# Kernel tuning notes

Measured on AMD Instinct MI355X. Metric: run time of the kernel, lower is better.

Reference implementation:

```python
import jax, jax.numpy as jnp
import numpy as np

N = 50000
E = 800000
IN_DIM, HID, OUT_DIM = 768, 256, 128
BN_EPS = 1e-5
NORM_EPS = 1e-12


def setup_inputs() -> dict:
    key = jax.random.key(0)
    ks = jax.random.split(key, 16)
    inp = {
        "x": jax.random.normal(ks[0], (N, IN_DIM), dtype=jnp.float32),
        "edge_index": jax.random.randint(ks[1], (2, E), 0, N, dtype=jnp.int64),
        "edge_weight": jax.random.uniform(ks[2], (E,), dtype=jnp.float32),
        # GCNConv weights (PyG: out = scatter(norm * (x @ W)[src]) + b)
        "W1": jax.random.normal(ks[3], (IN_DIM, HID), dtype=jnp.float32) * 0.02,
        "b1": jnp.zeros((HID,), jnp.float32),
        "W2": jax.random.normal(ks[4], (HID, HID), dtype=jnp.float32) * 0.02,
        "b2": jnp.zeros((HID,), jnp.float32),
        "W3": jax.random.normal(ks[5], (HID, OUT_DIM), dtype=jnp.float32) * 0.02,
        "b3": jnp.zeros((OUT_DIM,), jnp.float32),
        # BatchNorm (eval mode: running stats)
        "bn1_gamma": jnp.ones((HID,), jnp.float32),
        "bn1_beta": jnp.zeros((HID,), jnp.float32),
        "bn1_mean": jax.random.normal(ks[6], (HID,), dtype=jnp.float32) * 0.1,
        "bn1_var": jax.random.uniform(ks[7], (HID,), dtype=jnp.float32) + 0.5,
        "bn2_gamma": jnp.ones((HID,), jnp.float32),
        "bn2_beta": jnp.zeros((HID,), jnp.float32),
        "bn2_mean": jax.random.normal(ks[8], (HID,), dtype=jnp.float32) * 0.1,
        "bn2_var": jax.random.uniform(ks[9], (HID,), dtype=jnp.float32) + 0.5,
    }
    return inp


def _gcn_norm(edge_index, edge_weight, n):
    # add self loops with weight 1 (PyG GCNConv default)
    src = jnp.concatenate([edge_index[0], jnp.arange(n, dtype=edge_index.dtype)])
    dst = jnp.concatenate([edge_index[1], jnp.arange(n, dtype=edge_index.dtype)])
    ew = jnp.concatenate([edge_weight, jnp.ones((n,), edge_weight.dtype)])
    deg = jax.ops.segment_sum(ew, dst, num_segments=n)  # [N]
    dis = jnp.where(deg > 0, jax.lax.rsqrt(deg), 0.0)
    norm = dis[src] * ew * dis[dst]  # [E+N]
    return src, dst, norm


def _gcn_conv(h, W, b, src, dst, norm, n):
    h = h @ W                                  # [N, F_out]
    msg = h[src] * norm[:, None]               # gather + scale, [E+N, F_out]
    out = jax.ops.segment_sum(msg, dst, num_segments=n)  # scatter-add
    return out + b


def _bn_eval(h, gamma, beta, mean, var):
    return (h - mean) * jax.lax.rsqrt(var + BN_EPS) * gamma + beta


def reference(x, edge_index, edge_weight,
              W1, b1, W2, b2, W3, b3,
              bn1_gamma, bn1_beta, bn1_mean, bn1_var,
              bn2_gamma, bn2_beta, bn2_mean, bn2_var):
    n = x.shape[0]
    src, dst, norm = _gcn_norm(edge_index, edge_weight, n)
    h = _gcn_conv(x, W1, b1, src, dst, norm, n)
    h = jax.nn.relu(_bn_eval(h, bn1_gamma, bn1_beta, bn1_mean, bn1_var))
    h = _gcn_conv(h, W2, b2, src, dst, norm, n)
    h = jax.nn.relu(_bn_eval(h, bn2_gamma, bn2_beta, bn2_mean, bn2_var))
    h = _gcn_conv(h, W3, b3, src, dst, norm, n)
    # F.normalize(x, p=2, dim=1): x / max(||x||, eps)
    nrm = jnp.sqrt(jnp.sum(h * h, axis=1, keepdims=True))
    return h / jnp.maximum(nrm, NORM_EPS)
```

## Files before the change

kernel.cpp:

```cpp
#include <hip/hip_runtime.h>
#include <cstddef>

#define NN 50000
#define EE 800000
#define NB 196

typedef __attribute__((ext_vector_type(8))) _Float16 f16x8;
typedef __attribute__((ext_vector_type(4))) _Float16 f16x4;
typedef __attribute__((ext_vector_type(2))) _Float16 f16x2;
typedef __attribute__((ext_vector_type(4))) float f32x4;

__device__ __forceinline__ unsigned pk2h(float a, float b) {
  auto h = __builtin_amdgcn_cvt_pkrtz(a, b);
  return __builtin_bit_cast(unsigned, h);
}

__global__ void k_zero_off(int* __restrict__ off) {
  int i = blockIdx.x * 256 + threadIdx.x;
  if (i <= NN) off[i] = 0;
}

__global__ void k_count(const int* __restrict__ src, const int* __restrict__ dst,
                        int* __restrict__ off) {
  int e = blockIdx.x * 256 + threadIdx.x;
  if (e < EE) {
    int s = src[e], d = dst[e];
    if (s >= 0 && s < NN && d >= 0 && d < NN) atomicAdd(&off[d], 1);
  }
}

__global__ void k_scanA(int* __restrict__ off, int* __restrict__ bsum) {
  __shared__ int sh[256];
  int t = threadIdx.x;
  int idx = blockIdx.x * 256 + t;
  int v = (idx < NN) ? off[idx] : 0;
  sh[t] = v;
  __syncthreads();
  for (int d = 1; d < 256; d <<= 1) {
    int x = (t >= d) ? sh[t - d] : 0;
    __syncthreads();
    sh[t] += x;
    __syncthreads();
  }
  if (idx < NN) off[idx] = sh[t] - v;
  if (t == 255) bsum[blockIdx.x] = sh[255];
}

__global__ void k_scanB(int* __restrict__ bsum, int* __restrict__ bpre,
                        int* __restrict__ off) {
  __shared__ int sh[256];
  int t = threadIdx.x;
  int v = (t < NB) ? bsum[t] : 0;
  sh[t] = v;
  __syncthreads();
  for (int d = 1; d < 256; d <<= 1) {
    int x = (t >= d) ? sh[t - d] : 0;
    __syncthreads();
    sh[t] += x;
    __syncthreads();
  }
  if (t < NB) bpre[t] = sh[t] - v;
  if (t == 255) off[NN] = sh[255];
}

__global__ void k_scanC(int* __restrict__ off, const int* __restrict__ bpre,
                        int* __restrict__ cursor) {
  int idx = blockIdx.x * 256 + threadIdx.x;
  if (idx < NN) {
    int o = off[idx] + bpre[blockIdx.x];
    off[idx] = o;
    cursor[idx] = o;
  }
}

__global__ void k_fill(const int* __restrict__ src, const int* __restrict__ dst,
                       const float* __restrict__ ew, int* __restrict__ cursor,
                       int* __restrict__ csrc, float* __restrict__ cew) {
  int e = blockIdx.x * 256 + threadIdx.x;
  if (e < EE) {
    int s = src[e], d = dst[e];
    if (s >= 0 && s < NN && d >= 0 && d < NN) {
      int p = atomicAdd(&cursor[d], 1);
      csrc[p] = s;
      cew[p] = ew[e];
    }
  }
}

__global__ void k_degdis(const int* __restrict__ off, const float* __restrict__ cew,
                         float* __restrict__ dis) {
  int i = blockIdx.x * 256 + threadIdx.x;
  if (i >= NN) return;
  int e0 = off[i], e1 = off[i + 1];
  float s = 1.0f;
  for (int e = e0; e < e1; ++e) s += cew[e];
  dis[i] = rsqrtf(s);
}

__global__ void k_affine(const float* __restrict__ g1, const float* __restrict__ be1,
                         const float* __restrict__ m1, const float* __restrict__ v1,
                         const float* __restrict__ g2, const float* __restrict__ be2,
                         const float* __restrict__ m2, const float* __restrict__ v2,
                         float* __restrict__ s1, float* __restrict__ u1,
                         float* __restrict__ s2, float* __restrict__ u2) {
  int f = threadIdx.x;
  float a1 = g1[f] * rsqrtf(v1[f] + 1e-5f);
  s1[f] = a1; u1[f] = be1[f] - m1[f] * a1;
  float a2 = g2[f] * rsqrtf(v2[f] + 1e-5f);
  s2[f] = a2; u2[f] = be2[f] - m2[f] * a2;
}

__global__ void k_wt(const float* __restrict__ W, _Float16* __restrict__ WT,
                     int K, int N) {
  int k = blockIdx.x * 256 + threadIdx.x;
  int n = blockIdx.y;
  if (k < K) WT[(size_t)n * K + k] = (_Float16)W[(size_t)k * N + n];
}

#define LDA 40
__global__ __launch_bounds__(256) void k_gemm_mfma(const void* __restrict__ Ain,
                                                   const _Float16* __restrict__ BT,
                                                   _Float16* __restrict__ C,
                                                   int M, int K, int Nout, int a_fp32) {
  __shared__ _Float16 As[128 * LDA];
  __shared__ _Float16 Bs[128 * LDA];
  const int tid = threadIdx.x;
  const int bm = blockIdx.y << 7;
  const int bn = blockIdx.x << 7;
  const int lane = tid & 63;
  const int wid = tid >> 6;
  const int wm = (wid & 1) << 6;
  const int wn = (wid >> 1) << 6;
  const int quad = lane >> 4;
  const int l16 = lane & 15;

  f32x4 acc[4][4] = {};

  for (int k0 = 0; k0 < K; k0 += 32) {
#pragma unroll
    for (int j = 0; j < 2; ++j) {
      int c = tid + (j << 8);
      int row = c >> 2, kc = c & 3;
      uint4 va = make_uint4(0, 0, 0, 0);
      int gr = bm + row;
      if (gr < M) {
        if (a_fp32) {
          const float* p = (const float*)Ain + (size_t)gr * K + k0 + (kc << 3);
          float4 f0 = *(const float4*)p;
          float4 f1 = *(const float4*)(p + 4);
          va.x = pk2h(f0.x, f0.y);
          va.y = pk2h(f0.z, f0.w);
          va.z = pk2h(f1.x, f1.y);
          va.w = pk2h(f1.z, f1.w);
        } else {
          va = *(const uint4*)((const _Float16*)Ain + (size_t)gr * K + k0 + (kc << 3));
        }
      }
      *(uint4*)&As[row * LDA + (kc << 3)] = va;
      uint4 vb = *(const uint4*)(BT + (size_t)(bn + row) * K + k0 + (kc << 3));
      *(uint4*)&Bs[row * LDA + (kc << 3)] = vb;
    }
    __syncthreads();
    f16x8 af[4], bfr[4];
#pragma unroll
    for (int mt = 0; mt < 4; ++mt)
      af[mt] = *(const f16x8*)&As[(wm + (mt << 4) + l16) * LDA + (quad << 3)];
#pragma unroll
    for (int nt = 0; nt < 4; ++nt)
      bfr[nt] = *(const f16x8*)&Bs[(wn + (nt << 4) + l16) * LDA + (quad << 3)];
#pragma unroll
    for (int mt = 0; mt < 4; ++mt)
#pragma unroll
      for (int nt = 0; nt < 4; ++nt)
        acc[mt][nt] = __builtin_amdgcn_mfma_f32_16x16x32_f16(af[mt], bfr[nt], acc[mt][nt], 0, 0, 0);
    __syncthreads();
  }

  const int rbase = bm + wm + (quad << 2);
#pragma unroll
  for (int mt = 0; mt < 4; ++mt) {
#pragma unroll
    for (int reg = 0; reg < 4; ++reg) {
      int r = rbase + (mt << 4) + reg;
      if (r < M) {
        _Float16* crow = C + (size_t)r * Nout + bn + wn + l16;
#pragma unroll
        for (int nt = 0; nt < 4; ++nt) crow[nt << 4] = (_Float16)acc[mt][nt][reg];
      }
    }
  }
}

__global__ __launch_bounds__(256) void k_agg256(const _Float16* __restrict__ hW,
                                                const float* __restrict__ dis,
                                                const float* __restrict__ b,
                                                const int* __restrict__ off,
                                                const int* __restrict__ csrc,
                                                const float* __restrict__ cew,
                                                const float* __restrict__ s,
                                                const float* __restrict__ u,
                                                _Float16* __restrict__ hout) {
  int i = (blockIdx.x << 2) + (threadIdx.x >> 6);
  if (i >= NN) return;
  int lane = threadIdx.x & 63;
  float di = dis[i];
  float4 bb = *(const float4*)(b + (lane << 2));
  f16x4 hv = *(const f16x4*)(hW + (size_t)i * 256 + (lane << 2));
  float d2 = di * di;
  float4 acc;
  acc.x = fmaf((float)hv.x, d2, bb.x);
  acc.y = fmaf((float)hv.y, d2, bb.y);
  acc.z = fmaf((float)hv.z, d2, bb.z);
  acc.w = fmaf((float)hv.w, d2, bb.w);
  int e0 = off[i], e1 = off[i + 1];
  int e = e0;
  for (; e + 3 < e1; e += 4) {
    int sa = csrc[e], sb = csrc[e + 1], sc = csrc[e + 2], sd = csrc[e + 3];
    float wa = dis[sa] * cew[e] * di;
    float wb = dis[sb] * cew[e + 1] * di;
    float wc = dis[sc] * cew[e + 2] * di;
    float wd = dis[sd] * cew[e + 3] * di;
    f16x4 ra = *(const f16x4*)(hW + (size_t)sa * 256 + (lane << 2));
    f16x4 rb = *(const f16x4*)(hW + (size_t)sb * 256 + (lane << 2));
    f16x4 rc = *(const f16x4*)(hW + (size_t)sc * 256 + (lane << 2));
    f16x4 rd = *(const f16x4*)(hW + (size_t)sd * 256 + (lane << 2));
    acc.x = fmaf((float)ra.x, wa, acc.x); acc.y = fmaf((float)ra.y, wa, acc.y);
    acc.z = fmaf((float)ra.z, wa, acc.z); acc.w = fmaf((float)ra.w, wa, acc.w);
    acc.x = fmaf((float)rb.x, wb, acc.x); acc.y = fmaf((float)rb.y, wb, acc.y);
    acc.z = fmaf((float)rb.z, wb, acc.z); acc.w = fmaf((float)rb.w, wb, acc.w);
    acc.x = fmaf((float)rc.x, wc, acc.x); acc.y = fmaf((float)rc.y, wc, acc.y);
    acc.z = fmaf((float)rc.z, wc, acc.z); acc.w = fmaf((float)rc.w, wc, acc.w);
    acc.x = fmaf((float)rd.x, wd, acc.x); acc.y = fmaf((float)rd.y, wd, acc.y);
    acc.z = fmaf((float)rd.z, wd, acc.z); acc.w = fmaf((float)rd.w, wd, acc.w);
  }
  for (; e < e1; ++e) {
    int sa = csrc[e];
    float wa = dis[sa] * cew[e] * di;
    f16x4 ra = *(const f16x4*)(hW + (size_t)sa * 256 + (lane << 2));
    acc.x = fmaf((float)ra.x, wa, acc.x); acc.y = fmaf((float)ra.y, wa, acc.y);
    acc.z = fmaf((float)ra.z, wa, acc.z); acc.w = fmaf((float)ra.w, wa, acc.w);
  }
  float4 sv = *(const float4*)(s + (lane << 2));
  float4 uv = *(const float4*)(u + (lane << 2));
  float r0 = fmaxf(fmaf(acc.x, sv.x, uv.x), 0.f);
  float r1 = fmaxf(fmaf(acc.y, sv.y, uv.y), 0.f);
  float r2 = fmaxf(fmaf(acc.z, sv.z, uv.z), 0.f);
  float r3 = fmaxf(fmaf(acc.w, sv.w, uv.w), 0.f);
  uint2 pk;
  pk.x = pk2h(r0, r1);
  pk.y = pk2h(r2, r3);
  *(uint2*)&hout[(size_t)i * 256 + (lane << 2)] = pk;
}

__global__ __launch_bounds__(256) void k_agg128_l2(const _Float16* __restrict__ hW,
                                                   const float* __restrict__ dis,
                                                   const float* __restrict__ b,
                                                   const int* __restrict__ off,
                                                   const int* __restrict__ csrc,
                                                   const float* __restrict__ cew,
                                                   float* __restrict__ out) {
  int i = (blockIdx.x << 2) + (threadIdx.x >> 6);
  if (i >= NN) return;
  int lane = threadIdx.x & 63;
  float di = dis[i];
  float2 bb = *(const float2*)(b + (lane << 1));
  f16x2 hv = *(const f16x2*)(hW + (size_t)i * 128 + (lane << 1));
  float d2 = di * di;
  float2 acc;
  acc.x = fmaf((float)hv.x, d2, bb.x);
  acc.y = fmaf((float)hv.y, d2, bb.y);
  int e0 = off[i], e1 = off[i + 1];
  int e = e0;
  for (; e + 3 < e1; e += 4) {
    int sa = csrc[e], sb = csrc[e + 1], sc = csrc[e + 2], sd = csrc[e + 3];
    float wa = dis[sa] * cew[e] * di;
    float wb = dis[sb] * cew[e + 1] * di;
    float wc = dis[sc] * cew[e + 2] * di;
    float wd = dis[sd] * cew[e + 3] * di;
    f16x2 ra = *(const f16x2*)(hW + (size_t)sa * 128 + (lane << 1));
    f16x2 rb = *(const f16x2*)(hW + (size_t)sb * 128 + (lane << 1));
    f16x2 rc = *(const f16x2*)(hW + (size_t)sc * 128 + (lane << 1));
    f16x2 rd = *(const f16x2*)(hW + (size_t)sd * 128 + (lane << 1));
    acc.x = fmaf((float)ra.x, wa, acc.x); acc.y = fmaf((float)ra.y, wa, acc.y);
    acc.x = fmaf((float)rb.x, wb, acc.x); acc.y = fmaf((float)rb.y, wb, acc.y);
    acc.x = fmaf((float)rc.x, wc, acc.x); acc.y = fmaf((float)rc.y, wc, acc.y);
    acc.x = fmaf((float)rd.x, wd, acc.x); acc.y = fmaf((float)rd.y, wd, acc.y);
  }
  for (; e < e1; ++e) {
    int sa = csrc[e];
    float wa = dis[sa] * cew[e] * di;
    f16x2 ra = *(const f16x2*)(hW + (size_t)sa * 128 + (lane << 1));
    acc.x = fmaf((float)ra.x, wa, acc.x); acc.y = fmaf((float)ra.y, wa, acc.y);
  }
  float ss = fmaf(acc.x, acc.x, acc.y * acc.y);
#pragma unroll
  for (int o = 32; o > 0; o >>= 1) ss += __shfl_xor(ss, o, 64);
  float sc2 = 1.0f / fmaxf(sqrtf(ss), 1e-12f);
  acc.x *= sc2;
  acc.y *= sc2;
  *(float2*)(out + (size_t)i * 128 + (lane << 1)) = acc;
}

extern "C" void kernel_launch(void* const* d_in, const int* in_sizes, int n_in,
                              void* d_out, int out_size, void* d_ws, size_t ws_size,
                              hipStream_t stream) {
  const size_t OFF_CUR = 50176, OFF_BS = 100352, OFF_BP = 100608;
  const size_t OFF_CS = 100864, OFF_CW = 900864, OFF_DIS = 1700864;
  const size_t OFF_AFF = 1751040, OFF_HW = 1752064;
  const size_t OFF_HB = OFF_HW + (size_t)NN * 256;
  const size_t OFF_WT1 = OFF_HB + (size_t)NN * 128;
  const size_t OFF_WT2 = OFF_WT1 + 768 * 256 / 2;
  const size_t OFF_WT3 = OFF_WT2 + 256 * 256 / 2;
  const size_t WS_UNITS = OFF_WT3 + 256 * 128 / 2 + 256;
  if (ws_size < WS_UNITS * 4) return;

  const float* x  = (const float*)d_in[0];
  const int* ei   = (const int*)d_in[1];
  const float* ew = (const float*)d_in[2];
  const float* W1 = (const float*)d_in[3];
  const float* b1 = (const float*)d_in[4];
  const float* W2 = (const float*)d_in[5];
  const float* b2 = (const float*)d_in[6];
  const float* W3 = (const float*)d_in[7];
  const float* b3 = (const float*)d_in[8];
  const float* g1 = (const float*)d_in[9];
  const float* be1 = (const float*)d_in[10];
  const float* m1 = (const float*)d_in[11];
  const float* v1 = (const float*)d_in[12];
  const float* g2 = (const float*)d_in[13];
  const float* be2 = (const float*)d_in[14];
  const float* m2 = (const float*)d_in[15];
  const float* v2 = (const float*)d_in[16];
  float* out = (float*)d_out;
  const int* src = ei;
  const int* dstp = ei + EE;

  int* wsi = (int*)d_ws;
  float* wsf = (float*)d_ws;
  int* off = wsi;
  int* cursor = wsi + OFF_CUR;
  int* bsum = wsi + OFF_BS;
  int* bpre = wsi + OFF_BP;
  int* csrc = wsi + OFF_CS;
  float* cew = wsf + OFF_CW;
  float* dis = wsf + OFF_DIS;
  float* s1 = wsf + OFF_AFF;
  float* u1 = s1 + 256;
  float* s2 = u1 + 256;
  float* u2 = s2 + 256;
  _Float16* hW = (_Float16*)(wsf + OFF_HW);
  _Float16* hb = (_Float16*)(wsi + OFF_HB);
  _Float16* wT1 = (_Float16*)(wsi + OFF_WT1);
  _Float16* wT2 = (_Float16*)(wsi + OFF_WT2);
  _Float16* wT3 = (_Float16*)(wsi + OFF_WT3);

  dim3 b256(256);
  const int EB = (EE + 255) / 256;
  k_zero_off<<<NB, b256, 0, stream>>>(off);
  k_count<<<EB, b256, 0, stream>>>(src, dstp, off);
  k_scanA<<<NB, b256, 0, stream>>>(off, bsum);
  k_scanB<<<1, b256, 0, stream>>>(bsum, bpre, off);
  k_scanC<<<NB, b256, 0, stream>>>(off, bpre, cursor);
  k_fill<<<EB, b256, 0, stream>>>(src, dstp, ew, cursor, csrc, cew);
  k_degdis<<<NB, b256, 0, stream>>>(off, cew, dis);
  k_affine<<<1, b256, 0, stream>>>(g1, be1, m1, v1, g2, be2, m2, v2, s1, u1, s2, u2);
  k_wt<<<dim3(3, 256), b256, 0, stream>>>(W1, wT1, 768, 256);
  k_wt<<<dim3(1, 256), b256, 0, stream>>>(W2, wT2, 256, 256);
  k_wt<<<dim3(1, 128), b256, 0, stream>>>(W3, wT3, 256, 128);

  const int GM = (NN + 127) / 128;
  const int AGB = (NN + 3) / 4;
  k_gemm_mfma<<<dim3(2, GM), b256, 0, stream>>>(x, wT1, hW, NN, 768, 256, 1);
  k_agg256<<<AGB, b256, 0, stream>>>(hW, dis, b1, off, csrc, cew, s1, u1, hb);
  k_gemm_mfma<<<dim3(2, GM), b256, 0, stream>>>(hb, wT2, hW, NN, 256, 256, 0);
  k_agg256<<<AGB, b256, 0, stream>>>(hW, dis, b2, off, csrc, cew, s2, u2, hb);
  k_gemm_mfma<<<dim3(1, GM), b256, 0, stream>>>(hb, wT3, hW, NN, 256, 128, 0);
  k_agg128_l2<<<AGB, b256, 0, stream>>>(hW, dis, b3, off, csrc, cew, out);
}
```

Baseline: 633.2 us.

## Halve GEMM M-tile and prefetch next K-slice into registers

The MFMA GEMM tile shrinks from 128x128 to 64x128 rows per block, doubling the grid so more blocks are resident. The main loop also becomes software-pipelined: the next K-slice of A and B is loaded into registers while MFMAs run on the current LDS tile, then stored to LDS after a barrier. The aim is to hide global-load latency and raise occupancy. The cost is an extra barrier per iteration, less B-tile reuse per block, and more global traffic for B.

```diff
diff --git a/kernel.cpp b/kernel.cpp
--- a/kernel.cpp
+++ b/kernel.cpp
@@ -122,63 +122,92 @@
                                                    const _Float16* __restrict__ BT,
                                                    _Float16* __restrict__ C,
                                                    int M, int K, int Nout, int a_fp32) {
-  __shared__ _Float16 As[128 * LDA];
+  __shared__ _Float16 As[64 * LDA];
   __shared__ _Float16 Bs[128 * LDA];
   const int tid = threadIdx.x;
-  const int bm = blockIdx.y << 7;
+  const int bm = blockIdx.y << 6;
   const int bn = blockIdx.x << 7;
   const int lane = tid & 63;
   const int wid = tid >> 6;
-  const int wm = (wid & 1) << 6;
+  const int wm = (wid & 1) << 5;
   const int wn = (wid >> 1) << 6;
   const int quad = lane >> 4;
   const int l16 = lane & 15;
 
-  f32x4 acc[4][4] = {};
-
-  for (int k0 = 0; k0 < K; k0 += 32) {
-#pragma unroll
-    for (int j = 0; j < 2; ++j) {
-      int c = tid + (j << 8);
-      int row = c >> 2, kc = c & 3;
-      uint4 va = make_uint4(0, 0, 0, 0);
-      int gr = bm + row;
-      if (gr < M) {
+  const int srow = tid >> 2, skc = tid & 3;
+  const int agr = bm + srow;
+  const int aok = (agr < M);
+  const _Float16* brow0 = BT + (size_t)(bn + srow) * K + (skc << 3);
+  const _Float16* brow1 = BT + (size_t)(bn + 64 + srow) * K + (skc << 3);
+
+  f32x4 acc[2][4] = {};
+  uint4 ra, rb0, rb1;
+
+  const int T = K >> 5;
+
+  {
+    ra = make_uint4(0, 0, 0, 0);
+    if (aok) {
+      if (a_fp32) {
+        const float* p = (const float*)Ain + (size_t)agr * K + (skc << 3);
+        float4 f0 = *(const float4*)p;
+        float4 f1 = *(const float4*)(p + 4);
+        ra.x = pk2h(f0.x, f0.y); ra.y = pk2h(f0.z, f0.w);
+        ra.z = pk2h(f1.x, f1.y); ra.w = pk2h(f1.z, f1.w);
+      } else {
+        ra = *(const uint4*)((const _Float16*)Ain + (size_t)agr * K + (skc << 3));
+      }
+    }
+    rb0 = *(const uint4*)brow0;
+    rb1 = *(const uint4*)brow1;
+  }
+  *(uint4*)&As[srow * LDA + (skc << 3)] = ra;
+  *(uint4*)&Bs[srow * LDA + (skc << 3)] = rb0;
+  *(uint4*)&Bs[(64 + srow) * LDA + (skc << 3)] = rb1;
+  __syncthreads();
+
+  for (int t = 0; t < T; ++t) {
+    if (t + 1 < T) {
+      int k0 = (t + 1) << 5;
+      ra = make_uint4(0, 0, 0, 0);
+      if (aok) {
         if (a_fp32) {
-          const float* p = (const float*)Ain + (size_t)gr * K + k0 + (kc << 3);
+          const float* p = (const float*)Ain + (size_t)agr * K + k0 + (skc << 3);
           float4 f0 = *(const float4*)p;
           float4 f1 = *(const float4*)(p + 4);
-          va.x = pk2h(f0.x, f0.y);
-          va.y = pk2h(f0.z, f0.w);
-          va.z = pk2h(f1.x, f1.y);
-          va.w = pk2h(f1.z, f1.w);
+          ra.x = pk2h(f0.x, f0.y); ra.y = pk2h(f0.z, f0.w);
+          ra.z = pk2h(f1.x, f1.y); ra.w = pk2h(f1.z, f1.w);
         } else {
-          va = *(const uint4*)((const _Float16*)Ain + (size_t)gr * K + k0 + (kc << 3));
+          ra = *(const uint4*)((const _Float16*)Ain + (size_t)agr * K + k0 + (skc << 3));
         }
       }
-      *(uint4*)&As[row * LDA + (kc << 3)] = va;
-      uint4 vb = *(const uint4*)(BT + (size_t)(bn + row) * K + k0 + (kc << 3));
-      *(uint4*)&Bs[row * LDA + (kc << 3)] = vb;
+      rb0 = *(const uint4*)(brow0 + k0);
+      rb1 = *(const uint4*)(brow1 + k0);
     }
-    __syncthreads();
-    f16x8 af[4], bfr[4];
-#pragma unroll
-    for (int mt = 0; mt < 4; ++mt)
+    f16x8 af[2], bfr[4];
+#pragma unroll
+    for (int mt = 0; mt < 2; ++mt)
       af[mt] = *(const f16x8*)&As[(wm + (mt << 4) + l16) * LDA + (quad << 3)];
 #pragma unroll
     for (int nt = 0; nt < 4; ++nt)
       bfr[nt] = *(const f16x8*)&Bs[(wn + (nt << 4) + l16) * LDA + (quad << 3)];
 #pragma unroll
-    for (int mt = 0; mt < 4; ++mt)
+    for (int mt = 0; mt < 2; ++mt)
 #pragma unroll
       for (int nt = 0; nt < 4; ++nt)
         acc[mt][nt] = __builtin_amdgcn_mfma_f32_16x16x32_f16(af[mt], bfr[nt], acc[mt][nt], 0, 0, 0);
     __syncthreads();
+    if (t + 1 < T) {
+      *(uint4*)&As[srow * LDA + (skc << 3)] = ra;
+      *(uint4*)&Bs[srow * LDA + (skc << 3)] = rb0;
+      *(uint4*)&Bs[(64 + srow) * LDA + (skc << 3)] = rb1;
+    }
+    __syncthreads();
   }
 
   const int rbase = bm + wm + (quad << 2);
 #pragma unroll
-  for (int mt = 0; mt < 4; ++mt) {
+  for (int mt = 0; mt < 2; ++mt) {
 #pragma unroll
     for (int reg = 0; reg < 4; ++reg) {
       int r = rbase + (mt << 4) + reg;
@@ -368,7 +397,7 @@
   k_wt<<<dim3(1, 256), b256, 0, stream>>>(W2, wT2, 256, 256);
   k_wt<<<dim3(1, 128), b256, 0, stream>>>(W3, wT3, 256, 128);
 
-  const int GM = (NN + 127) / 128;
+  const int GM = (NN + 63) / 64;
   const int AGB = (NN + 3) / 4;
   k_gemm_mfma<<<dim3(2, GM), b256, 0, stream>>>(x, wT1, hW, NN, 768, 256, 1);
   k_agg256<<<AGB, b256, 0, stream>>>(hW, dis, b1, off, csrc, cew, s1, u1, hb);
```

Measured after the change: 602.3 us. 1.05x faster.

## Double-buffer GEMM shared tiles with register prefetch and shrink M tile to 64

Applied to the files above, without the earlier changes.

The MFMA GEMM now uses double-buffered shared-memory tiles. Global loads for the next K-slice are issued into registers before the current slice is computed and written to the other buffer afterwards, so load latency overlaps with MFMA work. The M tile shrinks from 128 to 64 rows, which doubles the block count and raises occupancy. The fp32/fp16 A path is now a template parameter instead of a runtime flag. In exchange, each block reuses the B tile across fewer rows, so more B traffic is re-read from L2, and more registers are held for the prefetch.

```diff
diff --git a/kernel.cpp b/kernel.cpp
--- a/kernel.cpp
+++ b/kernel.cpp
@@ -118,67 +118,108 @@
 }
 
 #define LDA 40
-__global__ __launch_bounds__(256) void k_gemm_mfma(const void* __restrict__ Ain,
-                                                   const _Float16* __restrict__ BT,
-                                                   _Float16* __restrict__ C,
-                                                   int M, int K, int Nout, int a_fp32) {
-  __shared__ _Float16 As[128 * LDA];
-  __shared__ _Float16 Bs[128 * LDA];
+template <int A32>
+__global__ __launch_bounds__(256) void k_gemm(const void* __restrict__ Ain,
+                                              const _Float16* __restrict__ BT,
+                                              _Float16* __restrict__ C,
+                                              int M, int K, int Nout) {
+  __shared__ _Float16 As[2][64 * LDA];
+  __shared__ _Float16 Bs[2][128 * LDA];
   const int tid = threadIdx.x;
-  const int bm = blockIdx.y << 7;
+  const int bm = blockIdx.y << 6;
   const int bn = blockIdx.x << 7;
   const int lane = tid & 63;
   const int wid = tid >> 6;
-  const int wm = (wid & 1) << 6;
+  const int wm = (wid & 1) << 5;
   const int wn = (wid >> 1) << 6;
   const int quad = lane >> 4;
   const int l16 = lane & 15;
 
-  f32x4 acc[4][4] = {};
-
-  for (int k0 = 0; k0 < K; k0 += 32) {
-#pragma unroll
-    for (int j = 0; j < 2; ++j) {
-      int c = tid + (j << 8);
-      int row = c >> 2, kc = c & 3;
-      uint4 va = make_uint4(0, 0, 0, 0);
-      int gr = bm + row;
-      if (gr < M) {
-        if (a_fp32) {
-          const float* p = (const float*)Ain + (size_t)gr * K + k0 + (kc << 3);
-          float4 f0 = *(const float4*)p;
-          float4 f1 = *(const float4*)(p + 4);
-          va.x = pk2h(f0.x, f0.y);
-          va.y = pk2h(f0.z, f0.w);
-          va.z = pk2h(f1.x, f1.y);
-          va.w = pk2h(f1.z, f1.w);
-        } else {
-          va = *(const uint4*)((const _Float16*)Ain + (size_t)gr * K + k0 + (kc << 3));
-        }
-      }
-      *(uint4*)&As[row * LDA + (kc << 3)] = va;
-      uint4 vb = *(const uint4*)(BT + (size_t)(bn + row) * K + k0 + (kc << 3));
-      *(uint4*)&Bs[row * LDA + (kc << 3)] = vb;
+  const int srow = tid >> 2, skc = tid & 3;
+  const int agr = bm + srow;
+  const int aok = (agr < M);
+  const _Float16* ap16 = (const _Float16*)Ain + (size_t)agr * K + (skc << 3);
+  const float* ap32 = (const float*)Ain + (size_t)agr * K + (skc << 3);
+  const _Float16* bp0 = BT + (size_t)(bn + srow) * K + (skc << 3);
+  const _Float16* bp1 = BT + (size_t)(bn + 64 + srow) * K + (skc << 3);
+
+  f32x4 acc[2][4] = {};
+
+  uint4 a16_0, a16_1;
+  float4 a32lo_0, a32hi_0, a32lo_1, a32hi_1;
+  uint4 b0_0, b1_0, b0_1, b1_1;
+
+#define ISSUE(S, k0)                                                        \
+  do {                                                                      \
+    if (A32) {                                                              \
+      if (aok) {                                                            \
+        a32lo_##S = *(const float4*)(ap32 + (k0));                          \
+        a32hi_##S = *(const float4*)(ap32 + (k0) + 4);                      \
+      } else {                                                              \
+        a32lo_##S = make_float4(0.f, 0.f, 0.f, 0.f);                       \
+        a32hi_##S = make_float4(0.f, 0.f, 0.f, 0.f);                       \
+      }                                                                     \
+    } else {                                                                \
+      a16_##S = aok ? *(const uint4*)(ap16 + (k0)) : make_uint4(0, 0, 0, 0);\
+    }                                                                       \
+    b0_##S = *(const uint4*)(bp0 + (k0));                                   \
+    b1_##S = *(const uint4*)(bp1 + (k0));                                   \
+  } while (0)
+
+#define COMMIT(S, buf)                                                      \
+  do {                                                                      \
+    uint4 va;                                                               \
+    if (A32) {                                                              \
+      va.x = pk2h(a32lo_##S.x, a32lo_##S.y);                                \
+      va.y = pk2h(a32lo_##S.z, a32lo_##S.w);                                \
+      va.z = pk2h(a32hi_##S.x, a32hi_##S.y);                                \
+      va.w = pk2h(a32hi_##S.z, a32hi_##S.w);                                \
+    } else {                                                                \
+      va = a16_##S;                                                         \
+    }                                                                       \
+    *(uint4*)&As[buf][srow * LDA + (skc << 3)] = va;                        \
+    *(uint4*)&Bs[buf][srow * LDA + (skc << 3)] = b0_##S;                    \
+    *(uint4*)&Bs[buf][(64 + srow) * LDA + (skc << 3)] = b1_##S;             \
+  } while (0)
+
+#define COMPUTE(buf)                                                        \
+  do {                                                                      \
+    f16x8 af[2], bfr[4];                                                    \
+    _Pragma("unroll") for (int mt = 0; mt < 2; ++mt)                        \
+        af[mt] = *(const f16x8*)&As[buf][(wm + (mt << 4) + l16) * LDA + (quad << 3)]; \
+    _Pragma("unroll") for (int nt = 0; nt < 4; ++nt)                        \
+        bfr[nt] = *(const f16x8*)&Bs[buf][(wn + (nt << 4) + l16) * LDA + (quad << 3)]; \
+    _Pragma("unroll") for (int mt = 0; mt < 2; ++mt)                        \
+        _Pragma("unroll") for (int nt = 0; nt < 4; ++nt)                    \
+            acc[mt][nt] = __builtin_amdgcn_mfma_f32_16x16x32_f16(af[mt], bfr[nt], acc[mt][nt], 0, 0, 0); \
+  } while (0)
+
+  const int T = K >> 5;
+
+  ISSUE(0, 0);
+  COMMIT(0, 0);
+  if (T > 1) ISSUE(1, 32);
+  __syncthreads();
+
+  for (int t = 0; t < T; t += 2) {
+    if (t + 2 < T) ISSUE(0, (t + 2) << 5);
+    COMPUTE(0);
+    if (t + 1 < T) COMMIT(1, 1);
+    __syncthreads();
+    if (t + 1 < T) {
+      if (t + 3 < T) ISSUE(1, (t + 3) << 5);
+      COMPUTE(1);
+      if (t + 2 < T) COMMIT(0, 0);
+      __syncthreads();
     }
-    __syncthreads();
-    f16x8 af[4], bfr[4];
-#pragma unroll
-    for (int mt = 0; mt < 4; ++mt)
-      af[mt] = *(const f16x8*)&As[(wm + (mt << 4) + l16) * LDA + (quad << 3)];
-#pragma unroll
-    for (int nt = 0; nt < 4; ++nt)
-      bfr[nt] = *(const f16x8*)&Bs[(wn + (nt << 4) + l16) * LDA + (quad << 3)];
-#pragma unroll
-    for (int mt = 0; mt < 4; ++mt)
-#pragma unroll
-      for (int nt = 0; nt < 4; ++nt)
-        acc[mt][nt] = __builtin_amdgcn_mfma_f32_16x16x32_f16(af[mt], bfr[nt], acc[mt][nt], 0, 0, 0);
-    __syncthreads();
-  }
+  }
+#undef ISSUE
+#undef COMMIT
+#undef COMPUTE
 
   const int rbase = bm + wm + (quad << 2);
 #pragma unroll
-  for (int mt = 0; mt < 4; ++mt) {
+  for (int mt = 0; mt < 2; ++mt) {
 #pragma unroll
     for (int reg = 0; reg < 4; ++reg) {
       int r = rbase + (mt << 4) + reg;
@@ -368,12 +409,12 @@
   k_wt<<<dim3(1, 256), b256, 0, stream>>>(W2, wT2, 256, 256);
   k_wt<<<dim3(1, 128), b256, 0, stream>>>(W3, wT3, 256, 128);
 
-  const int GM = (NN + 127) / 128;
+  const int GM = (NN + 63) / 64;
   const int AGB = (NN + 3) / 4;
-  k_gemm_mfma<<<dim3(2, GM), b256, 0, stream>>>(x, wT1, hW, NN, 768, 256, 1);
+  k_gemm<1><<<dim3(2, GM), b256, 0, stream>>>(x, wT1, hW, NN, 768, 256);
   k_agg256<<<AGB, b256, 0, stream>>>(hW, dis, b1, off, csrc, cew, s1, u1, hb);
-  k_gemm_mfma<<<dim3(2, GM), b256, 0, stream>>>(hb, wT2, hW, NN, 256, 256, 0);
+  k_gemm<0><<<dim3(2, GM), b256, 0, stream>>>(hb, wT2, hW, NN, 256, 256);
   k_agg256<<<AGB, b256, 0, stream>>>(hW, dis, b2, off, csrc, cew, s2, u2, hb);
-  k_gemm_mfma<<<dim3(1, GM), b256, 0, stream>>>(hb, wT3, hW, NN, 256, 128, 0);
+  k_gemm<0><<<dim3(1, GM), b256, 0, stream>>>(hb, wT3, hW, NN, 256, 128);
   k_agg128_l2<<<AGB, b256, 0, stream>>>(hW, dis, b3, off, csrc, cew, out);
 }
```

Measured after the change: 608.8 us. -3.9%, faster.

## Replace LDS-tiled GEMM with register-direct double-buffered MFMA loads

Applied to the files above, without the earlier changes.

The GEMM drops shared-memory staging and its barriers. Each wave now loads its A and B fragments directly from global memory into registers, with two-stage software double-buffering, and computes a 32x64 tile per wave (128x64 per block). The fp32/fp16 A path becomes a template parameter. This removes the LDS round-trip and __syncthreads, but B and A are reloaded from global/L2 by each wave with less reuse, and the grid doubles in the N dimension, which re-reads x across more blocks.

```diff
diff --git a/kernel.cpp b/kernel.cpp
--- a/kernel.cpp
+++ b/kernel.cpp
@@ -117,73 +117,90 @@
   if (k < K) WT[(size_t)n * K + k] = (_Float16)W[(size_t)k * N + n];
 }
 
-#define LDA 40
-__global__ __launch_bounds__(256) void k_gemm_mfma(const void* __restrict__ Ain,
-                                                   const _Float16* __restrict__ BT,
-                                                   _Float16* __restrict__ C,
-                                                   int M, int K, int Nout, int a_fp32) {
-  __shared__ _Float16 As[128 * LDA];
-  __shared__ _Float16 Bs[128 * LDA];
+template <int A32>
+__global__ __launch_bounds__(256) void k_gemm(const void* __restrict__ Ain,
+                                              const _Float16* __restrict__ BT,
+                                              _Float16* __restrict__ C,
+                                              int M, int K, int Nout) {
   const int tid = threadIdx.x;
-  const int bm = blockIdx.y << 7;
-  const int bn = blockIdx.x << 7;
   const int lane = tid & 63;
   const int wid = tid >> 6;
-  const int wm = (wid & 1) << 6;
-  const int wn = (wid >> 1) << 6;
+  const int bm = (blockIdx.y << 7) + (wid << 5);
+  const int bn = blockIdx.x << 6;
   const int quad = lane >> 4;
   const int l16 = lane & 15;
 
-  f32x4 acc[4][4] = {};
-
-  for (int k0 = 0; k0 < K; k0 += 32) {
+  const int r0 = bm + l16, r1 = bm + 16 + l16;
+  const size_t a0 = (size_t)(r0 < M ? r0 : 0) * K + (quad << 3);
+  const size_t a1 = (size_t)(r1 < M ? r1 : 0) * K + (quad << 3);
+  const float* ap32_0 = (const float*)Ain + a0;
+  const float* ap32_1 = (const float*)Ain + a1;
+  const _Float16* ap16_0 = (const _Float16*)Ain + a0;
+  const _Float16* ap16_1 = (const _Float16*)Ain + a1;
+  const _Float16* bp0 = BT + (size_t)(bn + l16) * K + (quad << 3);
+  const _Float16* bp1 = BT + (size_t)(bn + 16 + l16) * K + (quad << 3);
+  const _Float16* bp2 = BT + (size_t)(bn + 32 + l16) * K + (quad << 3);
+  const _Float16* bp3 = BT + (size_t)(bn + 48 + l16) * K + (quad << 3);
+
+  f32x4 acc[2][4] = {};
+
+  f16x8 af0_0, af1_0, bf0_0, bf1_0, bf2_0, bf3_0;
+  f16x8 af0_1, af1_1, bf0_1, bf1_1, bf2_1, bf3_1;
+
+#define LOADF(S, k0)                                                          \
+  do {                                                                        \
+    if (A32) {                                                                \
+      const float* p0 = ap32_0 + (k0);                                        \
+      const float* p1 = ap32_1 + (k0);                                        \
+      float4 u0 = *(const float4*)p0, v0 = *(const float4*)(p0 + 4);          \
+      float4 u1 = *(const float4*)p1, v1 = *(const float4*)(p1 + 4);          \
+      af0_##S = __builtin_bit_cast(f16x8,                                     \
+          make_uint4(pk2h(u0.x, u0.y), pk2h(u0.z, u0.w),                      \
+                     pk2h(v0.x, v0.y), pk2h(v0.z, v0.w)));                    \
+      af1_##S = __builtin_bit_cast(f16x8,                                     \
+          make_uint4(pk2h(u1.x, u1.y), pk2h(u1.z, u1.w),                      \
+                     pk2h(v1.x, v1.y), pk2h(v1.z, v1.w)));                    \
+    } else {                                                                  \
+      af0_##S = *(const f16x8*)(ap16_0 + (k0));                               \
+      af1_##S = *(const f16x8*)(ap16_1 + (k0));                               \
+    }                                                                         \
+    bf0_##S = *(const f16x8*)(bp0 + (k0));                                    \
+    bf1_##S = *(const f16x8*)(bp1 + (k0));                                    \
+    bf2_##S = *(const f16x8*)(bp2 + (k0));                                    \
+    bf3_##S = *(const f16x8*)(bp3 + (k0));                                    \
+  } while (0)
+
+#define MSTEP(S)                                                              \
+  do {                                                                        \
+    acc[0][0] = __builtin_amdgcn_mfma_f32_16x16x32_f16(af0_##S, bf0_##S, acc[0][0], 0, 0, 0); \
+    acc[0][1] = __builtin_amdgcn_mfma_f32_16x16x32_f16(af0_##S, bf1_##S, acc[0][1], 0, 0, 0); \
+    acc[0][2] = __builtin_amdgcn_mfma_f32_16x16x32_f16(af0_##S, bf2_##S, acc[0][2], 0, 0, 0); \
+    acc[0][3] = __builtin_amdgcn_mfma_f32_16x16x32_f16(af0_##S, bf3_##S, acc[0][3], 0, 0, 0); \
+    acc[1][0] = __builtin_amdgcn_mfma_f32_16x16x32_f16(af1_##S, bf0_##S, acc[1][0], 0, 0, 0); \
+    acc[1][1] = __builtin_amdgcn_mfma_f32_16x16x32_f16(af1_##S, bf1_##S, acc[1][1], 0, 0, 0); \
+    acc[1][2] = __builtin_amdgcn_mfma_f32_16x16x32_f16(af1_##S, bf2_##S, acc[1][2], 0, 0, 0); \
+    acc[1][3] = __builtin_amdgcn_mfma_f32_16x16x32_f16(af1_##S, bf3_##S, acc[1][3], 0, 0, 0); \
+  } while (0)
+
+  const int T = K >> 5;
+  LOADF(0, 0);
+  for (int t = 0; t < T; t += 2) {
+    if (t + 1 < T) LOADF(1, (t + 1) << 5);
+    MSTEP(0);
+    if (t + 2 < T) LOADF(0, (t + 2) << 5);
+    if (t + 1 < T) MSTEP(1);
+  }
+#undef LOADF
+#undef MSTEP
+
+  const int rbase = bm + (quad << 2);
 #pragma unroll
-    for (int j = 0; j < 2; ++j) {
-      int c = tid + (j << 8);
-      int row = c >> 2, kc = c & 3;
-      uint4 va = make_uint4(0, 0, 0, 0);
-      int gr = bm + row;
-      if (gr < M) {
-        if (a_fp32) {
-          const float* p = (const float*)Ain + (size_t)gr * K + k0 + (kc << 3);
-          float4 f0 = *(const float4*)p;
-          float4 f1 = *(const float4*)(p + 4);
-          va.x = pk2h(f0.x, f0.y);
-          va.y = pk2h(f0.z, f0.w);
-          va.z = pk2h(f1.x, f1.y);
-          va.w = pk2h(f1.z, f1.w);
-        } else {
-          va = *(const uint4*)((const _Float16*)Ain + (size_t)gr * K + k0 + (kc << 3));
-        }
-      }
-      *(uint4*)&As[row * LDA + (kc << 3)] = va;
-      uint4 vb = *(const uint4*)(BT + (size_t)(bn + row) * K + k0 + (kc << 3));
-      *(uint4*)&Bs[row * LDA + (kc << 3)] = vb;
-    }
-    __syncthreads();
-    f16x8 af[4], bfr[4];
-#pragma unroll
-    for (int mt = 0; mt < 4; ++mt)
-      af[mt] = *(const f16x8*)&As[(wm + (mt << 4) + l16) * LDA + (quad << 3)];
-#pragma unroll
-    for (int nt = 0; nt < 4; ++nt)
-      bfr[nt] = *(const f16x8*)&Bs[(wn + (nt << 4) + l16) * LDA + (quad << 3)];
-#pragma unroll
-    for (int mt = 0; mt < 4; ++mt)
-#pragma unroll
-      for (int nt = 0; nt < 4; ++nt)
-        acc[mt][nt] = __builtin_amdgcn_mfma_f32_16x16x32_f16(af[mt], bfr[nt], acc[mt][nt], 0, 0, 0);
-    __syncthreads();
-  }
-
-  const int rbase = bm + wm + (quad << 2);
-#pragma unroll
-  for (int mt = 0; mt < 4; ++mt) {
+  for (int mt = 0; mt < 2; ++mt) {
 #pragma unroll
     for (int reg = 0; reg < 4; ++reg) {
       int r = rbase + (mt << 4) + reg;
       if (r < M) {
-        _Float16* crow = C + (size_t)r * Nout + bn + wn + l16;
+        _Float16* crow = C + (size_t)r * Nout + bn + l16;
 #pragma unroll
         for (int nt = 0; nt < 4; ++nt) crow[nt << 4] = (_Float16)acc[mt][nt][reg];
       }
@@ -370,10 +387,10 @@
 
   const int GM = (NN + 127) / 128;
   const int AGB = (NN + 3) / 4;
-  k_gemm_mfma<<<dim3(2, GM), b256, 0, stream>>>(x, wT1, hW, NN, 768, 256, 1);
+  k_gemm<1><<<dim3(4, GM), b256, 0, stream>>>(x, wT1, hW, NN, 768, 256);
   k_agg256<<<AGB, b256, 0, stream>>>(hW, dis, b1, off, csrc, cew, s1, u1, hb);
-  k_gemm_mfma<<<dim3(2, GM), b256, 0, stream>>>(hb, wT2, hW, NN, 256, 256, 0);
+  k_gemm<0><<<dim3(4, GM), b256, 0, stream>>>(hb, wT2, hW, NN, 256, 256);
   k_agg256<<<AGB, b256, 0, stream>>>(hW, dis, b2, off, csrc, cew, s2, u2, hb);
-  k_gemm_mfma<<<dim3(1, GM), b256, 0, stream>>>(hb, wT3, hW, NN, 256, 128, 0);
+  k_gemm<0><<<dim3(2, GM), b256, 0, stream>>>(hb, wT3, hW, NN, 256, 128);
   k_agg128_l2<<<AGB, b256, 0, stream>>>(hW, dis, b3, off, csrc, cew, out);
 }
```

After: 698.2 us. +10.3%, slower.
